# Optimization experiments

Hardware: AMD Instinct MI355X
Metric: run time of the kernel (lower is better)

The kernel has to match this reference:

```python
import jax, jax.numpy as jnp
import numpy as np

B, S, D = 2, 2048, 1024
H, HD = 16, 64
WINDOW = 256
THETA = 10000.0
SCALING = 1.0


def _rope_tables(seq_len, dim, dtype):
    # Matches RotaryEmbedding: inv_freq over even indices, emb = cat((freqs, freqs), -1)
    inv_freq = 1.0 / (THETA ** (jnp.arange(0, dim, 2, dtype=jnp.float32) / dim))
    t = jnp.arange(seq_len, dtype=jnp.float32) / max(SCALING, 1e-6)
    freqs = jnp.outer(t, inv_freq)                      # [S, HD/2]
    emb = jnp.concatenate((freqs, freqs), axis=-1)      # [S, HD]
    return jnp.cos(emb).astype(dtype), jnp.sin(emb).astype(dtype)


def _rotate_half(x):
    # interleaved-pair rotation, faithful to the torch code
    x1 = x[..., ::2]
    x2 = x[..., 1::2]
    return jnp.stack((-x2, x1), axis=-1).reshape(x.shape)


def setup_inputs() -> dict:
    key = jax.random.key(0)
    ks = jax.random.split(key, 5)
    x = jax.random.normal(ks[0], (B, S, D), dtype=jnp.float32)
    w = lambda k: (jax.random.normal(k, (D, D), dtype=jnp.float32) * 0.02)
    return {"x": x, "Wq": w(ks[1]), "Wk": w(ks[2]), "Wv": w(ks[3]), "Wo": w(ks[4])}


def reference(x, Wq, Wk, Wv, Wo):
    bsz, seq_len, d_model = x.shape
    # QKV projections (torch Linear: y = x @ W.T), reshape to [B, H, S, HD]
    def proj(W):
        return (x @ W.T).reshape(bsz, seq_len, H, HD).transpose(0, 2, 1, 3)
    q, k, v = proj(Wq), proj(Wk), proj(Wv)

    cos, sin = _rope_tables(seq_len, HD, x.dtype)       # [S, HD]
    cos = cos[None, None]                               # [1,1,S,HD]
    sin = sin[None, None]
    q = q * cos + _rotate_half(q) * sin
    k = k * cos + _rotate_half(k) * sin

    scale = 1.0 / jnp.sqrt(jnp.asarray(HD, dtype=x.dtype))
    scores = jnp.einsum('bhqd,bhkd->bhqk', q, k) * scale  # [B,H,S,S]

    idx = jnp.arange(seq_len)
    allow = (idx[:, None] >= idx[None, :]) & (idx[:, None] - idx[None, :] < WINDOW)
    neg = jnp.asarray(jnp.finfo(scores.dtype).min, dtype=scores.dtype)
    scores = jnp.where(allow[None, None], scores, neg)

    attn = jax.nn.softmax(scores, axis=-1)
    y = jnp.einsum('bhqk,bhkd->bhqd', attn, v)           # [B,H,S,HD]
    y = y.transpose(0, 2, 1, 3).reshape(bsz, seq_len, d_model)
    return y @ Wo.T
```

## Files before the change

kernel.cpp:

```cpp
#include <hip/hip_runtime.h>
#include <math.h>
#include <stdint.h>

typedef unsigned short u16;
typedef __bf16 bf16x8 __attribute__((ext_vector_type(8)));
typedef float f32x4 __attribute__((ext_vector_type(4)));
typedef u16 u16x8 __attribute__((ext_vector_type(8)));

constexpr int Bb = 2, Ss = 2048, Dd = 1024, Hh = 16, Hd = 64, Win = 256;
constexpr int Mtot = Bb * Ss;

__device__ __forceinline__ u16 f2bf(float f) {
    uint32_t u = __float_as_uint(f);
    u += 0x7fff + ((u >> 16) & 1);
    return (u16)(u >> 16);
}

__device__ __forceinline__ void gload16(const void* g, void* l) {
    __builtin_amdgcn_global_load_lds(
        (const __attribute__((address_space(1))) uint32_t*)g,
        (__attribute__((address_space(3))) uint32_t*)l, 16, 0, 0);
}

__global__ void prep(const float* __restrict__ x,
                     const float* __restrict__ Wq, const float* __restrict__ Wk,
                     const float* __restrict__ Wv, const float* __restrict__ Wo,
                     u16* __restrict__ xb,
                     u16* __restrict__ wqb, u16* __restrict__ wkb,
                     u16* __restrict__ wvb, u16* __restrict__ wob,
                     float2* __restrict__ cs) {
    const int bid = blockIdx.x;
    if (bid < 8192) {
        const float* s;
        u16* d;
        int i;
        if (bid < 4096) {
            s = x; d = xb; i = bid * 256 + threadIdx.x;
        } else {
            int wsel = (bid - 4096) >> 10;
            i = ((bid - 4096) & 1023) * 256 + threadIdx.x;
            s = (wsel == 0) ? Wq : (wsel == 1) ? Wk : (wsel == 2) ? Wv : Wo;
            d = (wsel == 0) ? wqb : (wsel == 1) ? wkb : (wsel == 2) ? wvb : wob;
        }
        float4 v = reinterpret_cast<const float4*>(s)[i];
        ushort4 o;
        o.x = f2bf(v.x); o.y = f2bf(v.y); o.z = f2bf(v.z); o.w = f2bf(v.w);
        reinterpret_cast<ushort4*>(d)[i] = o;
    } else {
        int i = (bid - 8192) * 256 + threadIdx.x;
        int s = i >> 6, d = i & 63;
        float invf = powf(10000.0f, -(float)(d & 31) / 32.0f);
        float ang = (float)s * invf;
        float2 c; c.x = cosf(ang); c.y = sinf(ang);
        cs[i] = c;
    }
}

template <int MODE>
__global__ __launch_bounds__(512) void gemm_k(
    const u16* __restrict__ A,
    const u16* __restrict__ B0, const u16* __restrict__ B1, const u16* __restrict__ B2,
    void* __restrict__ C0, void* __restrict__ C1, void* __restrict__ C2,
    const float2* __restrict__ cs,
    int M, int N, int Kd)
{
    const u16* Bw = (blockIdx.z == 0) ? B0 : (blockIdx.z == 1) ? B1 : B2;
    void* C = (blockIdx.z == 0) ? C0 : (blockIdx.z == 1) ? C1 : C2;

    __shared__ u16 sA[128 * 32];
    __shared__ u16 sB[128 * 32];

    const int t = threadIdx.x, l = t & 63, w = t >> 6;
    const int wm = w >> 2, wn = w & 3;
    const int m0 = blockIdx.x * 128, n0 = blockIdx.y * 128;
    const int lr = l & 15, kg = l >> 4;

    const int sr = t >> 2;
    const int sg = (t & 3) ^ ((sr >> 1) & 3);

    f32x4 acc[4][2] = {};

    for (int k0 = 0; k0 < Kd; k0 += 32) {
        __syncthreads();
        gload16(A  + (size_t)(m0 + sr) * Kd + k0 + sg * 8, &sA[t * 8]);
        gload16(Bw + (size_t)(n0 + sr) * Kd + k0 + sg * 8, &sB[t * 8]);
        __syncthreads();

        bf16x8 af[4], bfr[2];
#pragma unroll
        for (int im = 0; im < 4; ++im) {
            int r = wm * 64 + im * 16 + lr;
            int slot = kg ^ ((r >> 1) & 3);
            af[im] = *reinterpret_cast<const bf16x8*>(&sA[r * 32 + slot * 8]);
        }
#pragma unroll
        for (int in = 0; in < 2; ++in) {
            int r = wn * 32 + in * 16 + lr;
            int slot = kg ^ ((r >> 1) & 3);
            bfr[in] = *reinterpret_cast<const bf16x8*>(&sB[r * 32 + slot * 8]);
        }
#pragma unroll
        for (int im = 0; im < 4; ++im)
#pragma unroll
            for (int in = 0; in < 2; ++in)
                acc[im][in] = __builtin_amdgcn_mfma_f32_16x16x32_bf16(
                    af[im], bfr[in], acc[im][in], 0, 0, 0);
    }

    const bool dorope = (MODE == 0) && (blockIdx.z < 2);
#pragma unroll
    for (int im = 0; im < 4; ++im) {
#pragma unroll
        for (int in = 0; in < 2; ++in) {
#pragma unroll
            for (int j = 0; j < 4; ++j) {
                int row = m0 + wm * 64 + im * 16 + kg * 4 + j;
                int col = n0 + wn * 32 + in * 16 + lr;
                float v = acc[im][in][j];
                if (MODE == 0) {
                    float vp = __shfl_xor(v, 1);
                    int b = row >> 11, s = row & 2047;
                    int h = col >> 6, d = col & 63;
                    float outv = v;
                    if (dorope) {
                        float2 c2 = cs[s * 64 + d];
                        outv = (col & 1) ? (v * c2.x + vp * c2.y)
                                         : (v * c2.x - vp * c2.y);
                    }
                    ((u16*)C)[(((size_t)(b * 16 + h)) * 2048 + s) * 64 + d] = f2bf(outv);
                } else {
                    ((float*)C)[(size_t)row * N + col] = v;
                }
            }
        }
    }
}

__global__ __launch_bounds__(256) void fattn(
    const u16* __restrict__ Qb, const u16* __restrict__ Kb,
    const u16* __restrict__ Vb, u16* __restrict__ O)
{
    __shared__ u16 sQ[64 * 64];
    __shared__ u16 sK[64 * 64];
    __shared__ u16 sVT[64 * 64];
    __shared__ u16 sP[4][16 * 64];

    const int t = threadIdx.x, l = t & 63, w = t >> 6;
    const int lo = l & 15, hi = l >> 4;
    const int qt = blockIdx.x, bh = blockIdx.y;
    const int q0 = qt * 64;

    const char* Qg = (const char*)(Qb + ((size_t)bh * Ss + q0) * 64);
#pragma unroll
    for (int p = 0; p < 2; ++p) {
        uint32_t x = (uint32_t)(w * 2 + p) * 1024 + l * 16;
        uint32_t sx = x ^ (((x >> 7) & 7) << 4);
        gload16(Qg + sx, (char*)sQ + x);
    }
    __syncthreads();

    bf16x8 qf[2];
#pragma unroll
    for (int ck = 0; ck < 2; ++ck) {
        uint32_t b = (uint32_t)(w * 16 + lo) * 128 + ck * 64 + hi * 16;
        b ^= ((lo & 7) << 4);
        qf[ck] = *reinterpret_cast<const bf16x8*>((const char*)sQ + b);
    }

    f32x4 o[4] = {};
    float mj[4], lj[4];
#pragma unroll
    for (int j = 0; j < 4; ++j) { mj[j] = -1e30f; lj[j] = 0.f; }

    const int jt0 = (qt >= 4) ? qt - 4 : 0;
    for (int jt = jt0; jt <= qt; ++jt) {
        __syncthreads();
        const char* Kg = (const char*)(Kb + ((size_t)bh * Ss + jt * 64) * 64);
#pragma unroll
        for (int p = 0; p < 2; ++p) {
            uint32_t x = (uint32_t)(w * 2 + p) * 1024 + l * 16;
            uint32_t sx = x ^ (((x >> 7) & 7) << 4);
            gload16(Kg + sx, (char*)sK + x);
        }
        const u16* Vg = Vb + ((size_t)bh * Ss + jt * 64) * 64;
#pragma unroll
        for (int p = 0; p < 2; ++p) {
            int c = p * 256 + t;
            int kr = c >> 3, dc = (c & 7) * 8;
            u16x8 vv = *reinterpret_cast<const u16x8*>(Vg + (size_t)kr * 64 + dc);
#pragma unroll
            for (int ii = 0; ii < 8; ++ii) {
                int d = dc + ii;
                uint32_t b = ((uint32_t)d * 128 + kr * 2) ^ (((uint32_t)(d & 7)) << 4);
                *(u16*)((char*)sVT + b) = vv[ii];
            }
        }
        __syncthreads();

        f32x4 s4[4] = {};
#pragma unroll
        for (int ck = 0; ck < 2; ++ck) {
#pragma unroll
            for (int nb = 0; nb < 4; ++nb) {
                uint32_t b = (uint32_t)(nb * 16 + lo) * 128 + ck * 64 + hi * 16;
                b ^= ((lo & 7) << 4);
                bf16x8 kf = *reinterpret_cast<const bf16x8*>((const char*)sK + b);
                s4[nb] = __builtin_amdgcn_mfma_f32_16x16x32_bf16(qf[ck], kf, s4[nb], 0, 0, 0);
            }
        }

        const int qbase = q0 + w * 16 + hi * 4;
#pragma unroll
        for (int nb = 0; nb < 4; ++nb) {
            int k = jt * 64 + nb * 16 + lo;
#pragma unroll
            for (int j = 0; j < 4; ++j) {
                int q = qbase + j;
                float v = s4[nb][j] * 0.125f;
                bool ok = (k <= q) && (q - k < Win);
                s4[nb][j] = ok ? v : -1e30f;
            }
        }

#pragma unroll
        for (int j = 0; j < 4; ++j) {
            float tm = fmaxf(fmaxf(s4[0][j], s4[1][j]), fmaxf(s4[2][j], s4[3][j]));
            tm = fmaxf(tm, __shfl_xor(tm, 1));
            tm = fmaxf(tm, __shfl_xor(tm, 2));
            tm = fmaxf(tm, __shfl_xor(tm, 4));
            tm = fmaxf(tm, __shfl_xor(tm, 8));
            float nm = fmaxf(fmaxf(mj[j], tm), -1e20f);
            float sc = __expf(mj[j] - nm);
            mj[j] = nm;
            lj[j] *= sc;
#pragma unroll
            for (int nb = 0; nb < 4; ++nb) o[nb][j] *= sc;
            float ps = 0.f;
#pragma unroll
            for (int nb = 0; nb < 4; ++nb) {
                float p = __expf(s4[nb][j] - nm);
                ps += p;
                s4[nb][j] = p;
            }
            lj[j] += ps;
        }

#pragma unroll
        for (int nb = 0; nb < 4; ++nb) {
#pragma unroll
            for (int j = 0; j < 4; ++j) {
                int r = hi * 4 + j;
                uint32_t b = ((uint32_t)r * 128 + (nb * 16 + lo) * 2) ^ (((uint32_t)(r & 7)) << 4);
                *(u16*)((char*)&sP[w][0] + b) = f2bf(s4[nb][j]);
            }
        }

#pragma unroll
        for (int ck = 0; ck < 2; ++ck) {
            uint32_t bp = ((uint32_t)lo * 128 + ck * 64 + hi * 16) ^ (((uint32_t)(lo & 7)) << 4);
            bf16x8 pa = *reinterpret_cast<const bf16x8*>((const char*)&sP[w][0] + bp);
#pragma unroll
            for (int nb = 0; nb < 4; ++nb) {
                uint32_t bb = ((uint32_t)(nb * 16 + lo) * 128 + ck * 64 + hi * 16) ^ (((uint32_t)(lo & 7)) << 4);
                bf16x8 vf = *reinterpret_cast<const bf16x8*>((const char*)sVT + bb);
                o[nb] = __builtin_amdgcn_mfma_f32_16x16x32_bf16(pa, vf, o[nb], 0, 0, 0);
            }
        }
    }

#pragma unroll
    for (int j = 0; j < 4; ++j) {
        float s = lj[j];
        s += __shfl_xor(s, 1);
        s += __shfl_xor(s, 2);
        s += __shfl_xor(s, 4);
        s += __shfl_xor(s, 8);
        lj[j] = 1.0f / s;
    }
    const int bq = bh >> 4, h = bh & 15;
#pragma unroll
    for (int nb = 0; nb < 4; ++nb) {
#pragma unroll
        for (int j = 0; j < 4; ++j) {
            int q = q0 + w * 16 + hi * 4 + j;
            int d = nb * 16 + lo;
            O[((size_t)(bq * Ss + q)) * Dd + h * 64 + d] = f2bf(o[nb][j] * lj[j]);
        }
    }
}

extern "C" void kernel_launch(void* const* d_in, const int* in_sizes, int n_in,
                              void* d_out, int out_size, void* d_ws, size_t ws_size,
                              hipStream_t stream) {
    const float* x  = (const float*)d_in[0];
    const float* Wq = (const float*)d_in[1];
    const float* Wk = (const float*)d_in[2];
    const float* Wv = (const float*)d_in[3];
    const float* Wo = (const float*)d_in[4];
    float* out = (float*)d_out;

    char* ws = (char*)d_ws;
    size_t off = 0;
    auto carve = [&](size_t bytes) -> char* {
        char* p = ws + off;
        off += (bytes + 255) & ~(size_t)255;
        return p;
    };
    float2* cs = (float2*)carve((size_t)Ss * 64 * 8);
    u16* xb  = (u16*)carve((size_t)Mtot * Dd * 2);
    u16* wqb = (u16*)carve((size_t)Dd * Dd * 2);
    u16* wkb = (u16*)carve((size_t)Dd * Dd * 2);
    u16* wvb = (u16*)carve((size_t)Dd * Dd * 2);
    u16* wob = (u16*)carve((size_t)Dd * Dd * 2);
    u16* Qbb = (u16*)carve((size_t)Mtot * Dd * 2);
    u16* Kbb = (u16*)carve((size_t)Mtot * Dd * 2);
    u16* Vbb = (u16*)carve((size_t)Mtot * Dd * 2);
    u16* attb = (u16*)carve((size_t)Mtot * Dd * 2);

    prep<<<8704, 256, 0, stream>>>(x, Wq, Wk, Wv, Wo,
                                   xb, wqb, wkb, wvb, wob, cs);

    gemm_k<0><<<dim3(Mtot / 128, Dd / 128, 3), 512, 0, stream>>>(
        xb, wqb, wkb, wvb, Qbb, Kbb, Vbb, cs, Mtot, Dd, Dd);

    fattn<<<dim3(Ss / 64, Bb * Hh), 256, 0, stream>>>(Qbb, Kbb, Vbb, attb);

    gemm_k<1><<<dim3(Mtot / 128, Dd / 128, 1), 512, 0, stream>>>(
        attb, wob, wob, wob, out, out, out, nullptr, Mtot, Dd, Dd);
}
```

Baseline: 105.4 us.

## Emit V pre-transposed from projection GEMM and async-load it in attention

The V projection block now computes Wv·xᵀ by swapping operands, so it writes V directly in a [b,h,d,s] transposed layout. The attention kernel can then fetch V tiles with the same swizzled global-to-LDS async loads used for K, replacing the per-element scalar transposing LDS stores. The trade-off is that the V output stores in the GEMM epilogue become strided scalar writes with poorer coalescing.

```diff
diff --git a/kernel.cpp b/kernel.cpp
--- a/kernel.cpp
+++ b/kernel.cpp
@@ -5,7 +5,6 @@
 typedef unsigned short u16;
 typedef __bf16 bf16x8 __attribute__((ext_vector_type(8)));
 typedef float f32x4 __attribute__((ext_vector_type(4)));
-typedef u16 u16x8 __attribute__((ext_vector_type(8)));
 
 constexpr int Bb = 2, Ss = 2048, Dd = 1024, Hh = 16, Hd = 64, Win = 256;
 constexpr int Mtot = Bb * Ss;
@@ -64,15 +63,27 @@
     const float2* __restrict__ cs,
     int M, int N, int Kd)
 {
-    const u16* Bw = (blockIdx.z == 0) ? B0 : (blockIdx.z == 1) ? B1 : B2;
-    void* C = (blockIdx.z == 0) ? C0 : (blockIdx.z == 1) ? C1 : C2;
+    const int z = blockIdx.z;
+    const u16* Am;
+    const u16* Bm;
+    int m0, n0;
+    if (MODE == 0 && z == 2) {
+        Am = B2; Bm = A;
+        m0 = blockIdx.y * 128;
+        n0 = blockIdx.x * 128;
+    } else {
+        Am = A;
+        Bm = (z == 0) ? B0 : (z == 1) ? B1 : B2;
+        m0 = blockIdx.x * 128;
+        n0 = blockIdx.y * 128;
+    }
+    void* C = (z == 0) ? C0 : (z == 1) ? C1 : C2;
 
     __shared__ u16 sA[128 * 32];
     __shared__ u16 sB[128 * 32];
 
     const int t = threadIdx.x, l = t & 63, w = t >> 6;
     const int wm = w >> 2, wn = w & 3;
-    const int m0 = blockIdx.x * 128, n0 = blockIdx.y * 128;
     const int lr = l & 15, kg = l >> 4;
 
     const int sr = t >> 2;
@@ -82,8 +93,8 @@
 
     for (int k0 = 0; k0 < Kd; k0 += 32) {
         __syncthreads();
-        gload16(A  + (size_t)(m0 + sr) * Kd + k0 + sg * 8, &sA[t * 8]);
-        gload16(Bw + (size_t)(n0 + sr) * Kd + k0 + sg * 8, &sB[t * 8]);
+        gload16(Am + (size_t)(m0 + sr) * Kd + k0 + sg * 8, &sA[t * 8]);
+        gload16(Bm + (size_t)(n0 + sr) * Kd + k0 + sg * 8, &sB[t * 8]);
         __syncthreads();
 
         bf16x8 af[4], bfr[2];
@@ -107,7 +118,6 @@
                     af[im], bfr[in], acc[im][in], 0, 0, 0);
     }
 
-    const bool dorope = (MODE == 0) && (blockIdx.z < 2);
 #pragma unroll
     for (int im = 0; im < 4; ++im) {
 #pragma unroll
@@ -118,16 +128,19 @@
                 int col = n0 + wn * 32 + in * 16 + lr;
                 float v = acc[im][in][j];
                 if (MODE == 0) {
-                    float vp = __shfl_xor(v, 1);
-                    int b = row >> 11, s = row & 2047;
-                    int h = col >> 6, d = col & 63;
-                    float outv = v;
-                    if (dorope) {
+                    if (z == 2) {
+                        int h = row >> 6, d = row & 63;
+                        int b = col >> 11, s = col & 2047;
+                        ((u16*)C)[((size_t)((b * 16 + h) * 64 + d)) * 2048 + s] = f2bf(v);
+                    } else {
+                        float vp = __shfl_xor(v, 1);
+                        int b = row >> 11, s = row & 2047;
+                        int h = col >> 6, d = col & 63;
                         float2 c2 = cs[s * 64 + d];
-                        outv = (col & 1) ? (v * c2.x + vp * c2.y)
-                                         : (v * c2.x - vp * c2.y);
+                        float outv = (col & 1) ? (v * c2.x + vp * c2.y)
+                                               : (v * c2.x - vp * c2.y);
+                        ((u16*)C)[(((size_t)(b * 16 + h)) * 2048 + s) * 64 + d] = f2bf(outv);
                     }
-                    ((u16*)C)[(((size_t)(b * 16 + h)) * 2048 + s) * 64 + d] = f2bf(outv);
                 } else {
                     ((float*)C)[(size_t)row * N + col] = v;
                 }
@@ -138,7 +151,7 @@
 
 __global__ __launch_bounds__(256) void fattn(
     const u16* __restrict__ Qb, const u16* __restrict__ Kb,
-    const u16* __restrict__ Vb, u16* __restrict__ O)
+    const u16* __restrict__ Vt, u16* __restrict__ O)
 {
     __shared__ u16 sQ[64 * 64];
     __shared__ u16 sK[64 * 64];
@@ -182,18 +195,12 @@
             uint32_t sx = x ^ (((x >> 7) & 7) << 4);
             gload16(Kg + sx, (char*)sK + x);
         }
-        const u16* Vg = Vb + ((size_t)bh * Ss + jt * 64) * 64;
+        const char* Vg = (const char*)(Vt + (size_t)bh * 64 * 2048 + (size_t)jt * 64);
 #pragma unroll
         for (int p = 0; p < 2; ++p) {
-            int c = p * 256 + t;
-            int kr = c >> 3, dc = (c & 7) * 8;
-            u16x8 vv = *reinterpret_cast<const u16x8*>(Vg + (size_t)kr * 64 + dc);
-#pragma unroll
-            for (int ii = 0; ii < 8; ++ii) {
-                int d = dc + ii;
-                uint32_t b = ((uint32_t)d * 128 + kr * 2) ^ (((uint32_t)(d & 7)) << 4);
-                *(u16*)((char*)sVT + b) = vv[ii];
-            }
+            uint32_t x = (uint32_t)(w * 2 + p) * 1024 + l * 16;
+            uint32_t sx = x ^ (((x >> 7) & 7) << 4);
+            gload16(Vg + (size_t)(x >> 7) * 4096 + (sx & 127), (char*)sVT + x);
         }
         __syncthreads();
 
@@ -314,16 +321,16 @@
     u16* wob = (u16*)carve((size_t)Dd * Dd * 2);
     u16* Qbb = (u16*)carve((size_t)Mtot * Dd * 2);
     u16* Kbb = (u16*)carve((size_t)Mtot * Dd * 2);
-    u16* Vbb = (u16*)carve((size_t)Mtot * Dd * 2);
+    u16* Vtb = (u16*)carve((size_t)Mtot * Dd * 2);
     u16* attb = (u16*)carve((size_t)Mtot * Dd * 2);
 
     prep<<<8704, 256, 0, stream>>>(x, Wq, Wk, Wv, Wo,
                                    xb, wqb, wkb, wvb, wob, cs);
 
     gemm_k<0><<<dim3(Mtot / 128, Dd / 128, 3), 512, 0, stream>>>(
-        xb, wqb, wkb, wvb, Qbb, Kbb, Vbb, cs, Mtot, Dd, Dd);
-
-    fattn<<<dim3(Ss / 64, Bb * Hh), 256, 0, stream>>>(Qbb, Kbb, Vbb, attb);
+        xb, wqb, wkb, wvb, Qbb, Kbb, Vtb, cs, Mtot, Dd, Dd);
+
+    fattn<<<dim3(Ss / 64, Bb * Hh), 256, 0, stream>>>(Qbb, Kbb, Vtb, attb);
 
     gemm_k<1><<<dim3(Mtot / 128, Dd / 128, 1), 512, 0, stream>>>(
         attb, wob, wob, wob, out, out, out, nullptr, Mtot, Dd, Dd);
```

Result: faster. 98.98 us (-6.1%).
